# Kernel tuning notes

Measured on AMD Instinct MI355X. Metric: run time of the kernel, lower is better.

The kernel has to match this reference:

```python
import jax, jax.numpy as jnp
import numpy as np

BN_EPS = 1e-5
ITER_N = 5

def _bn(x, gamma, beta, mean, var, axis):
    shape = [1] * x.ndim
    shape[axis] = -1
    r = lambda v: v.reshape(shape)
    return (x - r(mean)) * (r(gamma) / jnp.sqrt(r(var) + BN_EPS)) + r(beta)

def _covpool(x):
    # x: (B, d, M); MPNCOV CovpoolLayer: y = x @ I_hat @ x^T, I_hat = (1/M)I - (1/M^2)11^T
    M = x.shape[-1]
    I_hat = (-1.0 / (M * M)) * jnp.ones((M, M), x.dtype) + (1.0 / M) * jnp.eye(M, dtype=x.dtype)
    return jnp.einsum('bdm,mn,ben->bde', x, I_hat, x)

def _sqrtm_ns(A, iterN=ITER_N):
    # MPNCOV SqrtmLayer: trace-normalized Newton-Schulz iteration
    d = A.shape[-1]
    I3 = 3.0 * jnp.eye(d, dtype=A.dtype)
    normA = jnp.trace(A, axis1=1, axis2=2) / 3.0          # (B,)
    A_n = A / normA[:, None, None]
    ZY = 0.5 * (I3 - A_n)
    Y = A_n @ ZY
    Z = ZY
    for _ in range(iterN - 2):
        ZY = 0.5 * (I3 - Z @ Y)
        Y = Y @ ZY
        Z = ZY @ Z
    YZY = 0.5 * (Y @ (I3 - Z @ Y))
    return YZY * jnp.sqrt(normA)[:, None, None]

def setup_inputs() -> dict:
    key = jax.random.key(0)
    ks = jax.random.split(key, 12)
    B, C, H, W = 64, 1024, 16, 16
    D, R = 128, H * W  # att_dim, sp_reso
    return {
        'x': jax.random.normal(ks[0], (B, C, H, W), jnp.float32),
        'w_dr': jax.random.normal(ks[1], (D, C), jnp.float32) * 0.02,
        'b_dr': jax.random.normal(ks[2], (D,), jnp.float32) * 0.02,
        'bn1_gamma': jnp.ones((D,), jnp.float32),
        'bn1_beta': jnp.zeros((D,), jnp.float32),
        'bn1_mean': jax.random.normal(ks[3], (D,), jnp.float32) * 0.1,
        'bn1_var': jax.random.uniform(ks[4], (D,), jnp.float32, 0.5, 1.5),
        'bn2_gamma': jnp.ones((R,), jnp.float32),
        'bn2_beta': jnp.zeros((R,), jnp.float32),
        'bn2_mean': jax.random.normal(ks[5], (R,), jnp.float32) * 0.1,
        'bn2_var': jax.random.uniform(ks[6], (R,), jnp.float32, 0.5, 1.5),
        'rc_w': jax.random.normal(ks[7], (R,), jnp.float32) * 0.1 + 1.0,
        'rc_b': jax.random.normal(ks[8], (R,), jnp.float32) * 0.02,
        'fc_w': jax.random.normal(ks[9], (R, R * R), jnp.float32) * 0.004,
        'fc_b': jax.random.normal(ks[10], (R,), jnp.float32) * 0.02,
    }

def reference(x, w_dr, b_dr, bn1_gamma, bn1_beta, bn1_mean, bn1_var,
              bn2_gamma, bn2_beta, bn2_mean, bn2_var, rc_w, rc_b, fc_w, fc_b):
    B, C, H, W = x.shape
    # 1x1 dimension-reduction conv + BN + ReLU
    y = jnp.einsum('bchw,dc->bdhw', x, w_dr) + b_dr[None, :, None, None]
    y = jax.nn.relu(_bn(y, bn1_gamma, bn1_beta, bn1_mean, bn1_var, axis=1))
    # (B, D, HW) -> (B, HW, D): HW spatial positions as 'channels', D as samples
    y = y.reshape(B, -1, H * W).transpose(0, 2, 1)
    cov = _covpool(y)                  # (B, HW, HW)
    s = _sqrtm_ns(cov, ITER_N)         # (B, HW, HW)
    # row BN over first HW axis (channels of the (B, HW, HW, 1) view)
    s = _bn(s, bn2_gamma, bn2_beta, bn2_mean, bn2_var, axis=1)
    # grouped (depthwise) 1x1 row conv: per-row scale + bias
    s = s * rc_w[None, :, None] + rc_b[None, :, None]
    att = jax.nn.sigmoid(s.reshape(B, -1) @ fc_w.T + fc_b)   # (B, HW)
    att = att.reshape(B, 1, H, W)
    return x * att
```

## Files before the change

kernel.cpp:

```cpp
#include <hip/hip_runtime.h>

typedef unsigned short u16;
typedef unsigned int   u32;
typedef __attribute__((ext_vector_type(8))) short bf8;
typedef __attribute__((ext_vector_type(4))) float f4;
typedef __attribute__((ext_vector_type(16))) float f16f;

#define MFMA(a,b,c)   __builtin_amdgcn_mfma_f32_16x16x32_bf16(a,b,c,0,0,0)
#define MFMA32(a,b,c) __builtin_amdgcn_mfma_f32_32x32x16_bf16(a,b,c,0,0,0)

__device__ __forceinline__ u16 f2bf(float f){
  u32 u = __float_as_uint(f);
  u += 0x7fffu + ((u >> 16) & 1u);
  return (u16)(u >> 16);
}
__device__ __forceinline__ float bf2f(u16 h){ return __uint_as_float(((u32)h) << 16); }
__device__ __forceinline__ u32 pk2(float a, float b){ return (u32)f2bf(a) | ((u32)f2bf(b) << 16); }

__device__ __forceinline__ void glds16(const u16* g, u16* l){
  __builtin_amdgcn_global_load_lds((const __attribute__((address_space(1))) u32*)g,
                                   (__attribute__((address_space(3))) u32*)l, 16, 0, 0);
}

__device__ __forceinline__ bf8 ldsFrag(const char* m, int row0, int k0, int pitch){
  int l = threadIdx.x & 63;
  int r = row0 + (l & 15);
  int kb = ((k0 + ((l >> 4) << 3)) << 1) ^ ((r & 7) << 4);
  return *(const bf8*)(m + r * pitch + kb);
}
__device__ __forceinline__ void ldsPut(char* m, int row, int col, int pitch, u16 v){
  int kb = (col << 1) ^ ((row & 7) << 4);
  *(u16*)(m + row * pitch + kb) = v;
}

__device__ __forceinline__ bf8 fragNS(const char* m, int r0, int ks, int l){
  int r = r0 + (l & 31);
  int kb = ((ks << 5) + ((l >> 5) << 4)) ^ ((r & 15) << 4);
  return *(const bf8*)(m + r * 256 + kb);
}
__device__ __forceinline__ bf8 fragWT(const char* m, int r0, int ks, int l){
  int r = r0 + (l & 31);
  int kb = ((ks << 5) + ((l >> 5) << 4)) ^ ((r & 15) << 4);
  return *(const bf8*)(m + r * 512 + kb);
}
__device__ __forceinline__ char* nsAddr(char* m, int row, int col4){
  return m + row * 256 + ((col4 << 1) ^ ((row & 15) << 4));
}

__device__ __forceinline__ void mmPass(const char* A, const char* B, f16f (&acc)[2][2],
                                       int R0, int C0, int l){
  #pragma unroll
  for (int ks = 0; ks < 8; ++ks){
    bf8 a0 = fragNS(A, R0,      ks, l);
    bf8 a1 = fragNS(A, R0 + 32, ks, l);
    bf8 b0 = fragNS(B, C0,      ks, l);
    bf8 b1 = fragNS(B, C0 + 32, ks, l);
    acc[0][0] = MFMA32(a0, b0, acc[0][0]); acc[0][1] = MFMA32(a0, b1, acc[0][1]);
    acc[1][0] = MFMA32(a1, b0, acc[1][0]); acc[1][1] = MFMA32(a1, b1, acc[1][1]);
  }
}

__device__ __forceinline__ void writeTile(char* D, const f16f (&acc)[2][2], int R0, int C0, int l,
                                          float scale, float dval, const uint2* adv){
  #pragma unroll
  for (int ri = 0; ri < 2; ++ri)
  #pragma unroll
  for (int ci = 0; ci < 2; ++ci)
  #pragma unroll
  for (int g = 0; g < 4; ++g){
    int srow = C0 + ci * 32 + (l & 31);
    int scol = R0 + ri * 32 + g * 8 + ((l >> 5) << 2);
    float v[4];
    #pragma unroll
    for (int q = 0; q < 4; ++q){
      float x = scale * acc[ri][ci][g * 4 + q];
      x += ((scol + q) == srow) ? dval : 0.f;
      v[q] = x;
    }
    if (adv){
      uint2 ad = adv[(ri * 2 + ci) * 4 + g];
      v[0] += 1.5f * bf2f((u16)ad.x);
      v[1] += 1.5f * bf2f((u16)(ad.x >> 16));
      v[2] += 1.5f * bf2f((u16)ad.y);
      v[3] += 1.5f * bf2f((u16)(ad.y >> 16));
    }
    *(uint2*)nsAddr(D, srow, scol) = make_uint2(pk2(v[0], v[1]), pk2(v[2], v[3]));
  }
}

__global__ __launch_bounds__(256) void k_prep(const float* __restrict__ wdr,
                                              float* __restrict__ logits,
                                              u16* __restrict__ prep){
  int i = blockIdx.x * 256 + threadIdx.x;
  if (i < 16384) logits[i] = 0.f;
  #pragma unroll
  for (int j = 0; j < 2; ++j){
    int e = i + j * 65536;
    int chunk = e >> 13, rem = e & 8191, d = rem >> 6, cb2 = rem & 63;
    int c = ((cb2 * 2) ^ ((d & 7) << 4)) >> 1;
    prep[e] = f2bf(wdr[d * 1024 + chunk * 64 + c]);
  }
}

__global__ __launch_bounds__(512) void k_conv(
    const u16* __restrict__ wprep, const float* __restrict__ x, const float* __restrict__ bdr,
    const float* __restrict__ g1, const float* __restrict__ be1,
    const float* __restrict__ m1, const float* __restrict__ v1,
    u16* __restrict__ Wg, u16* __restrict__ WTg){
  __shared__ union {
    struct { u16 A[2][8192]; u16 Bt[2][2048]; } s;
    struct { float y[128 * 33]; float musum[512]; float mu[32]; } e;
  } sm;
  int t = threadIdx.x;
  int b = blockIdx.x >> 3, hw0 = (blockIdx.x & 7) * 32;
  const float* xb = x + (size_t)b * 262144 + hw0;

  int w = t >> 6, l = t & 63;
  int d0 = (w >> 1) * 32, hh = (w & 1) * 16;
  int lc = l & 15, lr = (l >> 4) * 4;

  const f4 fz = {0.f, 0.f, 0.f, 0.f};
  f4 acc[2]; acc[0] = fz; acc[1] = fz;

  int cp = t >> 5, hwl = t & 31;
  int bo0 = (4 * cp) ^ ((hwl & 7) << 4);
  int bo1 = (4 * cp + 64) ^ ((hwl & 7) << 4);

  glds16(wprep + t * 8,        sm.s.A[0] + t * 8);
  glds16(wprep + 4096 + t * 8, sm.s.A[0] + 4096 + t * 8);
  glds16(wprep + 8192 + t * 8,        sm.s.A[1] + t * 8);
  glds16(wprep + 8192 + 4096 + t * 8, sm.s.A[1] + 4096 + t * 8);
  float br0 = xb[(size_t)(2 * cp)      * 256 + hwl];
  float br1 = xb[(size_t)(2 * cp + 1)  * 256 + hwl];
  float br2 = xb[(size_t)(2 * cp + 32) * 256 + hwl];
  float br3 = xb[(size_t)(2 * cp + 33) * 256 + hwl];

  #pragma unroll
  for (int k = 0; k < 16; ++k){
    if (k >= 1 && k < 15){
      const u16* src = wprep + (k + 1) * 8192;
      glds16(src + t * 8,        sm.s.A[(k + 1) & 1] + t * 8);
      glds16(src + 4096 + t * 8, sm.s.A[(k + 1) & 1] + 4096 + t * 8);
    }
    float nb0 = 0.f, nb1 = 0.f, nb2 = 0.f, nb3 = 0.f;
    if (k < 15){
      int c0 = (k + 1) * 64;
      nb0 = xb[(size_t)(c0 + 2 * cp)      * 256 + hwl];
      nb1 = xb[(size_t)(c0 + 2 * cp + 1)  * 256 + hwl];
      nb2 = xb[(size_t)(c0 + 2 * cp + 32) * 256 + hwl];
      nb3 = xb[(size_t)(c0 + 2 * cp + 33) * 256 + hwl];
    }
    __builtin_amdgcn_sched_barrier(0);
    if (k == 0)       asm volatile("s_waitcnt vmcnt(4)" ::: "memory");
    else if (k == 15) asm volatile("s_waitcnt vmcnt(0)" ::: "memory");
    else              asm volatile("s_waitcnt vmcnt(6)" ::: "memory");
    __builtin_amdgcn_sched_barrier(0);
    *(u32*)((char*)sm.s.Bt[k & 1] + hwl * 128 + bo0) = pk2(br0, br1);
    *(u32*)((char*)sm.s.Bt[k & 1] + hwl * 128 + bo1) = pk2(br2, br3);
    asm volatile("s_waitcnt lgkmcnt(0)" ::: "memory");
    __builtin_amdgcn_sched_barrier(0);
    __builtin_amdgcn_s_barrier();
    __builtin_amdgcn_sched_barrier(0);
    #pragma unroll
    for (int ks = 0; ks < 2; ++ks){
      int k0 = ks * 32;
      bf8 a0 = ldsFrag((const char*)sm.s.A[k & 1], d0,      k0, 128);
      bf8 a1 = ldsFrag((const char*)sm.s.A[k & 1], d0 + 16, k0, 128);
      bf8 b0 = ldsFrag((const char*)sm.s.Bt[k & 1], hh, k0, 128);
      acc[0] = MFMA(a0, b0, acc[0]);
      acc[1] = MFMA(a1, b0, acc[1]);
    }
    __builtin_amdgcn_sched_barrier(0);
    __builtin_amdgcn_s_barrier();
    __builtin_amdgcn_sched_barrier(0);
    br0 = nb0; br1 = nb1; br2 = nb2; br3 = nb3;
  }
  __syncthreads();

  #pragma unroll
  for (int i = 0; i < 2; ++i)
    #pragma unroll
    for (int r = 0; r < 4; ++r){
      int d = d0 + i * 16 + lr + r;
      float s1 = g1[d] * rsqrtf(v1[d] + 1e-5f);
      float t1 = (bdr[d] - m1[d]) * s1 + be1[d];
      int hwp = hh + lc;
      sm.e.y[d * 33 + hwp] = fmaxf(acc[i][r] * s1 + t1, 0.f);
    }
  __syncthreads();
  { int part = t >> 5, col = t & 31;
    float s = 0.f;
    #pragma unroll
    for (int i2 = 0; i2 < 8; ++i2) s += sm.e.y[(part * 8 + i2) * 33 + col];
    sm.e.musum[part * 32 + col] = s;
  }
  __syncthreads();
  if (t < 32){
    float m = 0.f;
    #pragma unroll
    for (int p = 0; p < 16; ++p) m += sm.e.musum[p * 32 + t];
    sm.e.mu[t] = m * (1.0f / 128.0f);
  }
  __syncthreads();
  const float ISM = 0.08838834764831845f;
  { int hwp = t >> 4, dc = (t & 15) * 8;
    float muv = sm.e.mu[hwp];
    u32 q[4];
    #pragma unroll
    for (int jj = 0; jj < 4; ++jj){
      float a = (sm.e.y[(dc + 2 * jj)     * 33 + hwp] - muv) * ISM;
      float c = (sm.e.y[(dc + 2 * jj + 1) * 33 + hwp] - muv) * ISM;
      q[jj] = pk2(a, c);
    }
    *(uint4*)(Wg + ((size_t)(b * 256 + hw0 + hwp) * 128 + dc)) = make_uint4(q[0], q[1], q[2], q[3]);
  }
  { int d = t >> 2, hc = (t & 3) * 8;
    u32 q[4];
    #pragma unroll
    for (int jj = 0; jj < 4; ++jj){
      int h0 = hc + 2 * jj, h1 = hc + 2 * jj + 1;
      float a = (sm.e.y[d * 33 + h0] - sm.e.mu[h0]) * ISM;
      float c = (sm.e.y[d * 33 + h1] - sm.e.mu[h1]) * ISM;
      q[jj] = pk2(a, c);
    }
    *(uint4*)(WTg + ((size_t)(b * 128 + d) * 256 + hw0 + hc)) = make_uint4(q[0], q[1], q[2], q[3]);
  }
}

extern __shared__ char smns[];
__global__ __launch_bounds__(512, 2) void k_ns(const u16* __restrict__ WT,
                                               u16* __restrict__ yf, float* __restrict__ normAg){
  int b = blockIdx.x, t = threadIdx.x;
  char* Yb = smns;
  char* Zb = smns + 32768;
  char* T1 = smns + 65536;
  char* T2 = smns + 98304;
  char* T3 = smns + 131072;
  char* WTl = smns + 65536;
  char* G   = T3;
  float* trp = (float*)smns;

  int w = t >> 6, l = t & 63;
  int wq = w & 3;
  int R0 = (wq >> 1) * 64, C0 = (wq & 1) * 64;

  { const u16* src = WT + (size_t)b * 32768;
    int row = t >> 2, q = t & 3;
    #pragma unroll
    for (int j = 0; j < 8; ++j) {
      int c16 = q + j * 4;
      bf8 v = *(const bf8*)(src + row * 256 + c16 * 8);
      int ph = c16 ^ (row & 15);
      *(bf8*)(WTl + row * 512 + ph * 16) = v;
    }
  }
  if (t == 0) *trp = 0.f;
  __syncthreads();

  int R0g = (w & 3) * 32, C0g = (w >> 2) * 64;
  const f16f fz16 = {};
  f16f gac[2]; gac[0] = fz16; gac[1] = fz16;
  #pragma unroll
  for (int ks = 0; ks < 16; ++ks){
    bf8 a  = fragWT(WTl, R0g,      ks, l);
    bf8 b0 = fragWT(WTl, C0g,      ks, l);
    bf8 b1 = fragWT(WTl, C0g + 32, ks, l);
    gac[0] = MFMA32(a, b0, gac[0]);
    gac[1] = MFMA32(a, b1, gac[1]);
  }
  float tp = 0.f;
  #pragma unroll
  for (int ci = 0; ci < 2; ++ci)
    #pragma unroll
    for (int e = 0; e < 16; ++e){
      int row = R0g + (e & 3) + 8 * (e >> 2) + ((l >> 5) << 2);
      int col = C0g + ci * 32 + (l & 31);
      if (row == col) tp += gac[ci][e];
    }
  #pragma unroll
  for (int off = 32; off > 0; off >>= 1) tp += __shfl_down(tp, off);
  if (l == 0) atomicAdd(trp, tp);
  __syncthreads();

  float normA = fmaxf(*trp / 3.0f, 1e-12f);
  if (t == 0) normAg[b] = normA;
  float inv = 1.0f / normA;
  #pragma unroll
  for (int ci = 0; ci < 2; ++ci)
    #pragma unroll
    for (int g = 0; g < 4; ++g){
      int srow = C0g + ci * 32 + (l & 31);
      int scol = R0g + g * 8 + ((l >> 5) << 2);
      float v0 = gac[ci][g * 4 + 0] * inv, v1 = gac[ci][g * 4 + 1] * inv;
      float v2 = gac[ci][g * 4 + 2] * inv, v3 = gac[ci][g * 4 + 3] * inv;
      *(uint2*)nsAddr(G, srow, scol) = make_uint2(pk2(v0, v1), pk2(v2, v3));
    }
  __syncthreads();

  bf8 gA[8], gB[8];
  #pragma unroll
  for (int ks = 0; ks < 8; ++ks){
    gA[ks] = fragNS(G, C0,      ks, l);
    gB[ks] = fragNS(G, C0 + 32, ks, l);
  }
  { int row = t >> 2, q4 = t & 3;
    #pragma unroll
    for (int j = 0; j < 4; ++j){
      int c16 = q4 * 4 + j;
      int ph = c16 ^ (row & 15);
      bf8 gg = *(const bf8*)(G + row * 256 + ph * 16);
      bf8 yv, zv;
      #pragma unroll
      for (int e = 0; e < 8; ++e){
        int col = c16 * 8 + e;
        float y = -0.5f * bf2f((u16)gg[e]) + ((col == row) ? 1.5f : 0.f);
        yv[e] = (short)f2bf(y);
        zv[e] = (col == row) ? (short)f2bf(-0.5f) : (short)0;
      }
      *(bf8*)(Yb + row * 256 + ph * 16) = yv;
      *(bf8*)(Zb + row * 256 + ph * 16) = zv;
    }
  }
  __syncthreads();

  float z0 = 1.5f;
  for (int it = 0; it < 4; ++it){
    {
      f16f acc[2][2]; acc[0][0] = fz16; acc[0][1] = fz16; acc[1][0] = fz16; acc[1][1] = fz16;
      const char* As = (w < 4) ? Zb : Yb;
      #pragma unroll
      for (int ks = 0; ks < 8; ++ks){
        bf8 a0 = fragNS(As, R0,      ks, l);
        bf8 a1 = fragNS(As, R0 + 32, ks, l);
        acc[0][0] = MFMA32(a0, gA[ks], acc[0][0]); acc[0][1] = MFMA32(a0, gB[ks], acc[0][1]);
        acc[1][0] = MFMA32(a1, gA[ks], acc[1][0]); acc[1][1] = MFMA32(a1, gB[ks], acc[1][1]);
      }
      writeTile((w < 4) ? T1 : T3, acc, R0, C0, l, 1.0f, (w < 4) ? z0 : 0.f, nullptr);
    }
    __syncthreads();

    uint2 adv[16];
    {
      const char* addsrc = (w < 4) ? Zb : Yb;
      #pragma unroll
      for (int ri = 0; ri < 2; ++ri)
      #pragma unroll
      for (int ci = 0; ci < 2; ++ci)
      #pragma unroll
      for (int g = 0; g < 4; ++g){
        int srow = C0 + ci * 32 + (l & 31);
        int scol = R0 + ri * 32 + g * 8 + ((l >> 5) << 2);
        adv[(ri * 2 + ci) * 4 + g] = *(const uint2*)nsAddr((char*)addsrc, srow, scol);
      }
      if (w < 4){
        f16f acc[2][2]; acc[0][0] = fz16; acc[0][1] = fz16; acc[1][0] = fz16; acc[1][1] = fz16;
        mmPass(T1, Yb, acc, R0, C0, l);
        writeTile(T2, acc, R0, C0, l, -0.5f, 0.f, nullptr);
      }
    }
    __syncthreads();

    if ((w >= 4) || (it < 3)){
      f16f acc[2][2]; acc[0][0] = fz16; acc[0][1] = fz16; acc[1][0] = fz16; acc[1][1] = fz16;
      const char* A3 = (w < 4) ? T2 : T3;
      const char* B3 = (w < 4) ? T1 : T2;
      mmPass(A3, B3, acc, R0, C0, l);
      writeTile((w < 4) ? Zb : Yb, acc, R0, C0, l, 1.0f, 0.f, adv);
    }
    __syncthreads();
    z0 *= 1.5f;
  }

  { int row = t >> 2, q = t & 3;
    u16* dst = yf + (size_t)b * 16384 + row * 128;
    #pragma unroll
    for (int j = 0; j < 4; ++j) {
      int c16 = q * 4 + j;
      int ph = c16 ^ (row & 15);
      *(bf8*)(dst + c16 * 8) = *(const bf8*)(Yb + row * 256 + ph * 16);
    }
  }
}

extern __shared__ char smex[];
__global__ __launch_bounds__(512) void k_expand(
    const u16* __restrict__ Wg, const u16* __restrict__ yf, const float* __restrict__ normAg,
    const float* __restrict__ g2, const float* __restrict__ be2, const float* __restrict__ m2,
    const float* __restrict__ v2, const float* __restrict__ rcw, const float* __restrict__ rcb,
    u16* __restrict__ sp){
  int blk = blockIdx.x, b = blk >> 2, iband = blk & 3;
  char* Bm = smex;
  char* Yl = smex + 65536;
  char* El = smex + 98304;
  int t = threadIdx.x;
  { const u16* src = Wg + (size_t)b * 32768;
    int row = t >> 1, q = t & 1;
    #pragma unroll
    for (int j = 0; j < 8; ++j) {
      int c16 = q + j * 2;
      bf8 v = *(const bf8*)(src + row * 128 + c16 * 8);
      int ph = c16 ^ (row & 7);
      *(bf8*)(Bm + row * 256 + ph * 16) = v;
    } }
  { const u16* src = yf + (size_t)b * 16384;
    int row = t >> 2, q = t & 3;
    #pragma unroll
    for (int j = 0; j < 4; ++j) {
      int c16 = q + j * 4;
      bf8 v = *(const bf8*)(src + row * 128 + c16 * 8);
      int ph = c16 ^ (row & 7);
      *(bf8*)(Yl + row * 256 + ph * 16) = v;
    } }
  __syncthreads();
  int w = t >> 6, l = t & 63, lc = l & 15, lr = (l >> 4) * 4;
  const f4 fz = {0.f, 0.f, 0.f, 0.f};
  { int r0 = (w >> 2) * 32, c0 = (w & 3) * 32;
    f4 acc[2][2];
    acc[0][0] = fz; acc[0][1] = fz; acc[1][0] = fz; acc[1][1] = fz;
    #pragma unroll
    for (int kk = 0; kk < 4; ++kk) {
      int k0 = kk * 32;
      bf8 a0 = ldsFrag(Bm, iband * 64 + r0,      k0, 256);
      bf8 a1 = ldsFrag(Bm, iband * 64 + r0 + 16, k0, 256);
      bf8 b0 = ldsFrag(Yl, c0,      k0, 256);
      bf8 b1 = ldsFrag(Yl, c0 + 16, k0, 256);
      acc[0][0] = MFMA(a0, b0, acc[0][0]); acc[0][1] = MFMA(a0, b1, acc[0][1]);
      acc[1][0] = MFMA(a1, b0, acc[1][0]); acc[1][1] = MFMA(a1, b1, acc[1][1]);
    }
    #pragma unroll
    for (int i = 0; i < 2; ++i)
      #pragma unroll
      for (int j = 0; j < 2; ++j)
        #pragma unroll
        for (int r = 0; r < 4; ++r)
          ldsPut(El, r0 + i * 16 + lr + r, c0 + j * 16 + lc, 256, f2bf(acc[i][j][r]));
  }
  __syncthreads();
  { float invs = rsqrtf(normAg[b]);
    int r0 = (w >> 2) * 32, c0 = (w & 3) * 64;
    f4 acc[2][4];
    #pragma unroll
    for (int i = 0; i < 2; ++i)
      #pragma unroll
      for (int j = 0; j < 4; ++j) acc[i][j] = fz;
    #pragma unroll
    for (int kk = 0; kk < 4; ++kk) {
      int k0 = kk * 32;
      bf8 a0 = ldsFrag(El, r0,      k0, 256);
      bf8 a1 = ldsFrag(El, r0 + 16, k0, 256);
      bf8 b0 = ldsFrag(Bm, c0,      k0, 256);
      bf8 b1 = ldsFrag(Bm, c0 + 16, k0, 256);
      bf8 b2 = ldsFrag(Bm, c0 + 32, k0, 256);
      bf8 b3 = ldsFrag(Bm, c0 + 48, k0, 256);
      acc[0][0] = MFMA(a0, b0, acc[0][0]); acc[0][1] = MFMA(a0, b1, acc[0][1]);
      acc[0][2] = MFMA(a0, b2, acc[0][2]); acc[0][3] = MFMA(a0, b3, acc[0][3]);
      acc[1][0] = MFMA(a1, b0, acc[1][0]); acc[1][1] = MFMA(a1, b1, acc[1][1]);
      acc[1][2] = MFMA(a1, b2, acc[1][2]); acc[1][3] = MFMA(a1, b3, acc[1][3]);
    }
    #pragma unroll
    for (int i = 0; i < 2; ++i)
      #pragma unroll
      for (int r = 0; r < 4; ++r) {
        int il = r0 + i * 16 + lr + r;
        int ig = iband * 64 + il;
        float bs = g2[ig] * rsqrtf(v2[ig] + 1e-5f);
        float al = bs * rcw[ig];
        float be = (be2[ig] - m2[ig] * bs) * rcw[ig] + rcb[ig];
        #pragma unroll
        for (int j = 0; j < 4; ++j) {
          int jg = c0 + j * 16 + lc;
          sp[(size_t)b * 65536 + ig * 256 + jg] = f2bf(acc[i][j][r] * invs * al + be);
        }
      }
  }
}

__global__ __launch_bounds__(256) void k_fc(const u16* __restrict__ sp,
                                            const float* __restrict__ fcw,
                                            float* __restrict__ partial){
  __shared__ char Bl[2][16384];
  int kc = blockIdx.x >> 2, rq = blockIdx.x & 3;
  int t = threadIdx.x, w = t >> 6, l = t & 63;
  int k0 = kc * 512, rbase = rq * 64;
  int br0 = (w & 1) * 32;
  int cr0 = (w >> 1) * 32;

  const f4 fz = {0.f, 0.f, 0.f, 0.f};
  f4 acc[2][2];
  acc[0][0] = fz; acc[0][1] = fz; acc[1][0] = fz; acc[1][1] = fz;

  float4 fbA[8], fbB[8];
  bf8 faA[8], faB[8];

  #define LOADB(S, FB) { \
    _Pragma("unroll") \
    for (int j = 0; j < 8; ++j){ \
      int fid = t + 256 * j; \
      int row = fid >> 5, c4 = fid & 31; \
      FB[j] = *(const float4*)(fcw + (size_t)(rbase + row) * 65536 + k0 + (S) * 128 + c4 * 4); \
    } }
  #define LOADA(S, FA) { \
    _Pragma("unroll") \
    for (int g = 0; g < 2; ++g) \
    _Pragma("unroll") \
    for (int ks = 0; ks < 4; ++ks) \
      FA[g * 4 + ks] = *(const bf8*)(sp + (size_t)(br0 + 16 * g + (l & 15)) * 65536 \
                                     + k0 + (S) * 128 + ks * 32 + (l >> 4) * 8); \
    }
  #define WRITEB(CUR, FB) { \
    _Pragma("unroll") \
    for (int j = 0; j < 8; ++j){ \
      int fid = t + 256 * j; \
      int row = fid >> 5, c4 = fid & 31; \
      int off = row * 256 + ((c4 * 8) ^ ((row & 7) << 4)); \
      *(uint2*)(&Bl[CUR][0] + off) = make_uint2(pk2(FB[j].x, FB[j].y), pk2(FB[j].z, FB[j].w)); \
    } }
  #define DOMFMA(CUR, FA) { \
    _Pragma("unroll") \
    for (int ks = 0; ks < 4; ++ks){ \
      bf8 b0 = ldsFrag(&Bl[CUR][0], cr0,      ks * 32, 256); \
      bf8 b1 = ldsFrag(&Bl[CUR][0], cr0 + 16, ks * 32, 256); \
      acc[0][0] = MFMA(FA[ks],     b0, acc[0][0]); \
      acc[0][1] = MFMA(FA[ks],     b1, acc[0][1]); \
      acc[1][0] = MFMA(FA[4 + ks], b0, acc[1][0]); \
      acc[1][1] = MFMA(FA[4 + ks], b1, acc[1][1]); \
    } }
  #define FENCE __builtin_amdgcn_sched_barrier(0)
  #define BARRIER { FENCE; __builtin_amdgcn_s_barrier(); FENCE; }

  LOADB(0, fbA); LOADA(0, faA);
  LOADB(1, fbB); LOADA(1, faB);

  FENCE; asm volatile("s_waitcnt vmcnt(16)" ::: "memory"); FENCE;
  WRITEB(0, fbA);
  asm volatile("s_waitcnt lgkmcnt(0)" ::: "memory");
  BARRIER;
  DOMFMA(0, faA);
  LOADB(2, fbA); LOADA(2, faA);
  BARRIER;
  FENCE; asm volatile("s_waitcnt vmcnt(16)" ::: "memory"); FENCE;
  WRITEB(1, fbB);
  asm volatile("s_waitcnt lgkmcnt(0)" ::: "memory");
  BARRIER;
  DOMFMA(1, faB);
  LOADB(3, fbB); LOADA(3, faB);
  BARRIER;
  FENCE; asm volatile("s_waitcnt vmcnt(16)" ::: "memory"); FENCE;
  WRITEB(0, fbA);
  asm volatile("s_waitcnt lgkmcnt(0)" ::: "memory");
  BARRIER;
  DOMFMA(0, faA);
  BARRIER;
  FENCE; asm volatile("s_waitcnt vmcnt(0)" ::: "memory"); FENCE;
  WRITEB(1, fbB);
  asm volatile("s_waitcnt lgkmcnt(0)" ::: "memory");
  BARRIER;
  DOMFMA(1, faB);

  #undef LOADB
  #undef LOADA
  #undef WRITEB
  #undef DOMFMA
  #undef FENCE
  #undef BARRIER

  float* pout = partial + (size_t)kc * 16384;
  #pragma unroll
  for (int g = 0; g < 2; ++g)
    #pragma unroll
    for (int j = 0; j < 2; ++j)
      #pragma unroll
      for (int q = 0; q < 4; ++q){
        int brow = br0 + g * 16 + ((l >> 4) << 2) + q;
        int rcol = rbase + cr0 + j * 16 + (l & 15);
        pout[brow * 256 + rcol] = acc[g][j][q];
      }
}

__global__ __launch_bounds__(256) void k_red(const float* __restrict__ partial,
                                             float* __restrict__ logits){
  int i = blockIdx.x * 256 + threadIdx.x;
  float s0 = 0.f, s1 = 0.f, s2 = 0.f, s3 = 0.f;
  #pragma unroll 8
  for (int kc = 0; kc < 128; kc += 4){
    s0 += partial[(size_t)(kc + 0) * 16384 + i];
    s1 += partial[(size_t)(kc + 1) * 16384 + i];
    s2 += partial[(size_t)(kc + 2) * 16384 + i];
    s3 += partial[(size_t)(kc + 3) * 16384 + i];
  }
  logits[i] = (s0 + s1) + (s2 + s3);
}

__global__ __launch_bounds__(256) void k_mul(const float* __restrict__ x,
                                             const float* __restrict__ logits,
                                             const float* __restrict__ fcb,
                                             float* __restrict__ out, int n4){
  int i = blockIdx.x * 256 + threadIdx.x;
  int str = gridDim.x * 256;
  for (; i < n4; i += str) {
    int e = i << 2;
    int b = e >> 18;
    int hw = e & 255;
    float4 xv = ((const float4*)x)[i];
    float4 lg = *(const float4*)(logits + (b << 8) + hw);
    float4 fb = *(const float4*)(fcb + hw);
    float4 o;
    o.x = xv.x / (1.f + expf(-(lg.x + fb.x)));
    o.y = xv.y / (1.f + expf(-(lg.y + fb.y)));
    o.z = xv.z / (1.f + expf(-(lg.z + fb.z)));
    o.w = xv.w / (1.f + expf(-(lg.w + fb.w)));
    ((float4*)out)[i] = o;
  }
}

extern "C" void kernel_launch(void* const* d_in, const int* in_sizes, int n_in,
                              void* d_out, int out_size, void* d_ws, size_t ws_size,
                              hipStream_t stream){
  const float* x   = (const float*)d_in[0];
  const float* wdr = (const float*)d_in[1];
  const float* bdr = (const float*)d_in[2];
  const float* g1  = (const float*)d_in[3];
  const float* be1 = (const float*)d_in[4];
  const float* m1  = (const float*)d_in[5];
  const float* v1  = (const float*)d_in[6];
  const float* g2  = (const float*)d_in[7];
  const float* be2 = (const float*)d_in[8];
  const float* m2  = (const float*)d_in[9];
  const float* v2  = (const float*)d_in[10];
  const float* rcw = (const float*)d_in[11];
  const float* rcb = (const float*)d_in[12];
  const float* fcw = (const float*)d_in[13];
  const float* fcb = (const float*)d_in[14];
  float* out = (float*)d_out;
  char* ws = (char*)d_ws;
  u16*   Wg  = (u16*)(ws);
  u16*   WTg = (u16*)(ws + (4u  << 20));
  u16*   yfg = (u16*)(ws + (8u  << 20));
  float* nAg = (float*)(ws + (10u << 20));
  u16*   wpr = (u16*)(ws + (10u << 20) + 4096);
  u16*   spg = (u16*)(ws + (11u << 20));
  float* lgt = (float*)(ws + (20u << 20));
  float* prt = (float*)(ws + (24u << 20));

  hipFuncSetAttribute((const void*)k_ns,     hipFuncAttributeMaxDynamicSharedMemorySize, 163840);
  hipFuncSetAttribute((const void*)k_expand, hipFuncAttributeMaxDynamicSharedMemorySize, 114688);

  k_prep  <<<256,  256, 0,      stream>>>(wdr, lgt, wpr);
  k_conv  <<<512,  512, 0,      stream>>>(wpr, x, bdr, g1, be1, m1, v1, Wg, WTg);
  k_ns    <<<64,   512, 163840, stream>>>(WTg, yfg, nAg);
  k_expand<<<256,  512, 114688, stream>>>(Wg, yfg, nAg, g2, be2, m2, v2, rcw, rcb, spg);
  k_fc    <<<512,  256, 0,      stream>>>(spg, fcw, prt);
  k_red   <<<64,   256, 0,      stream>>>(prt, lgt);
  k_mul   <<<2048, 256, 0,      stream>>>(x, lgt, fcb, out, 4194304);
}
```

Measured before the change: 115.3 us.

## Deepen conv weight/input prefetch pipeline and split NS matmul across all waves

The 1x1 conv kernel goes from a double-buffered weight stage to a four-slot LDS ring that prefetches three chunks ahead. The x-input register prefetch also moves to a three-deep rotation, so more global loads are in flight before each MFMA step; the vmcnt waits are retuned to match. In the Newton-Schulz kernel, the T1*Y product was computed only by waves 0-3. It is now split across all eight waves, each computing a 64x32 half-tile, which removes idle waves at that step. The cost is more LDS for the conv kernel, which may lower occupancy, and more live registers.

```diff
diff --git a/kernel.cpp b/kernel.cpp
--- a/kernel.cpp
+++ b/kernel.cpp
@@ -108,7 +108,7 @@
     const float* __restrict__ m1, const float* __restrict__ v1,
     u16* __restrict__ Wg, u16* __restrict__ WTg){
   __shared__ union {
-    struct { u16 A[2][8192]; u16 Bt[2][2048]; } s;
+    struct { u16 A[4][8192]; u16 Bt[2][2048]; } s;
     struct { float y[128 * 33]; float musum[512]; float mu[32]; } e;
   } sm;
   int t = threadIdx.x;
@@ -126,37 +126,44 @@
   int bo0 = (4 * cp) ^ ((hwl & 7) << 4);
   int bo1 = (4 * cp + 64) ^ ((hwl & 7) << 4);
 
-  glds16(wprep + t * 8,        sm.s.A[0] + t * 8);
-  glds16(wprep + 4096 + t * 8, sm.s.A[0] + 4096 + t * 8);
-  glds16(wprep + 8192 + t * 8,        sm.s.A[1] + t * 8);
-  glds16(wprep + 8192 + 4096 + t * 8, sm.s.A[1] + 4096 + t * 8);
-  float br0 = xb[(size_t)(2 * cp)      * 256 + hwl];
-  float br1 = xb[(size_t)(2 * cp + 1)  * 256 + hwl];
-  float br2 = xb[(size_t)(2 * cp + 32) * 256 + hwl];
-  float br3 = xb[(size_t)(2 * cp + 33) * 256 + hwl];
+  float br[3][4];
+  #pragma unroll
+  for (int j = 0; j < 3; ++j){
+    glds16(wprep + j * 8192 + t * 8,        sm.s.A[j] + t * 8);
+    glds16(wprep + j * 8192 + 4096 + t * 8, sm.s.A[j] + 4096 + t * 8);
+    __builtin_amdgcn_sched_barrier(0);
+    int c0 = j * 64;
+    br[j][0] = xb[(size_t)(c0 + 2 * cp)      * 256 + hwl];
+    br[j][1] = xb[(size_t)(c0 + 2 * cp + 1)  * 256 + hwl];
+    br[j][2] = xb[(size_t)(c0 + 2 * cp + 32) * 256 + hwl];
+    br[j][3] = xb[(size_t)(c0 + 2 * cp + 33) * 256 + hwl];
+    __builtin_amdgcn_sched_barrier(0);
+  }
 
   #pragma unroll
   for (int k = 0; k < 16; ++k){
-    if (k >= 1 && k < 15){
-      const u16* src = wprep + (k + 1) * 8192;
-      glds16(src + t * 8,        sm.s.A[(k + 1) & 1] + t * 8);
-      glds16(src + 4096 + t * 8, sm.s.A[(k + 1) & 1] + 4096 + t * 8);
-    }
-    float nb0 = 0.f, nb1 = 0.f, nb2 = 0.f, nb3 = 0.f;
-    if (k < 15){
-      int c0 = (k + 1) * 64;
-      nb0 = xb[(size_t)(c0 + 2 * cp)      * 256 + hwl];
-      nb1 = xb[(size_t)(c0 + 2 * cp + 1)  * 256 + hwl];
-      nb2 = xb[(size_t)(c0 + 2 * cp + 32) * 256 + hwl];
-      nb3 = xb[(size_t)(c0 + 2 * cp + 33) * 256 + hwl];
-    }
-    __builtin_amdgcn_sched_barrier(0);
-    if (k == 0)       asm volatile("s_waitcnt vmcnt(4)" ::: "memory");
-    else if (k == 15) asm volatile("s_waitcnt vmcnt(0)" ::: "memory");
-    else              asm volatile("s_waitcnt vmcnt(6)" ::: "memory");
-    __builtin_amdgcn_sched_barrier(0);
-    *(u32*)((char*)sm.s.Bt[k & 1] + hwl * 128 + bo0) = pk2(br0, br1);
-    *(u32*)((char*)sm.s.Bt[k & 1] + hwl * 128 + bo1) = pk2(br2, br3);
+    if (k <= 12){
+      const u16* src = wprep + (k + 3) * 8192;
+      glds16(src + t * 8,        sm.s.A[(k + 3) & 3] + t * 8);
+      glds16(src + 4096 + t * 8, sm.s.A[(k + 3) & 3] + 4096 + t * 8);
+    }
+    __builtin_amdgcn_sched_barrier(0);
+    if (k <= 12)      asm volatile("s_waitcnt vmcnt(14)" ::: "memory");
+    else if (k == 13) asm volatile("s_waitcnt vmcnt(12)" ::: "memory");
+    else if (k == 14) asm volatile("s_waitcnt vmcnt(6)" ::: "memory");
+    else              asm volatile("s_waitcnt vmcnt(0)" ::: "memory");
+    __builtin_amdgcn_sched_barrier(0);
+    *(u32*)((char*)sm.s.Bt[k & 1] + hwl * 128 + bo0) = pk2(br[k % 3][0], br[k % 3][1]);
+    *(u32*)((char*)sm.s.Bt[k & 1] + hwl * 128 + bo1) = pk2(br[k % 3][2], br[k % 3][3]);
+    __builtin_amdgcn_sched_barrier(0);
+    if (k <= 12){
+      int c0 = (k + 3) * 64;
+      br[k % 3][0] = xb[(size_t)(c0 + 2 * cp)      * 256 + hwl];
+      br[k % 3][1] = xb[(size_t)(c0 + 2 * cp + 1)  * 256 + hwl];
+      br[k % 3][2] = xb[(size_t)(c0 + 2 * cp + 32) * 256 + hwl];
+      br[k % 3][3] = xb[(size_t)(c0 + 2 * cp + 33) * 256 + hwl];
+    }
+    __builtin_amdgcn_sched_barrier(0);
     asm volatile("s_waitcnt lgkmcnt(0)" ::: "memory");
     __builtin_amdgcn_sched_barrier(0);
     __builtin_amdgcn_s_barrier();
@@ -164,8 +171,8 @@
     #pragma unroll
     for (int ks = 0; ks < 2; ++ks){
       int k0 = ks * 32;
-      bf8 a0 = ldsFrag((const char*)sm.s.A[k & 1], d0,      k0, 128);
-      bf8 a1 = ldsFrag((const char*)sm.s.A[k & 1], d0 + 16, k0, 128);
+      bf8 a0 = ldsFrag((const char*)sm.s.A[k & 3], d0,      k0, 128);
+      bf8 a1 = ldsFrag((const char*)sm.s.A[k & 3], d0 + 16, k0, 128);
       bf8 b0 = ldsFrag((const char*)sm.s.Bt[k & 1], hh, k0, 128);
       acc[0] = MFMA(a0, b0, acc[0]);
       acc[1] = MFMA(a1, b0, acc[1]);
@@ -173,7 +180,6 @@
     __builtin_amdgcn_sched_barrier(0);
     __builtin_amdgcn_s_barrier();
     __builtin_amdgcn_sched_barrier(0);
-    br0 = nb0; br1 = nb1; br2 = nb2; br3 = nb3;
   }
   __syncthreads();
 
@@ -352,10 +358,25 @@
         int scol = R0 + ri * 32 + g * 8 + ((l >> 5) << 2);
         adv[(ri * 2 + ci) * 4 + g] = *(const uint2*)nsAddr((char*)addsrc, srow, scol);
       }
-      if (w < 4){
-        f16f acc[2][2]; acc[0][0] = fz16; acc[0][1] = fz16; acc[1][0] = fz16; acc[1][1] = fz16;
-        mmPass(T1, Yb, acc, R0, C0, l);
-        writeTile(T2, acc, R0, C0, l, -0.5f, 0.f, nullptr);
+      int hC0 = C0 + ((w >> 2) << 5);
+      f16f a2[2]; a2[0] = fz16; a2[1] = fz16;
+      #pragma unroll
+      for (int ks = 0; ks < 8; ++ks){
+        bf8 a0 = fragNS(T1, R0,      ks, l);
+        bf8 a1 = fragNS(T1, R0 + 32, ks, l);
+        bf8 b0 = fragNS(Yb, hC0,     ks, l);
+        a2[0] = MFMA32(a0, b0, a2[0]);
+        a2[1] = MFMA32(a1, b0, a2[1]);
+      }
+      #pragma unroll
+      for (int ri = 0; ri < 2; ++ri)
+      #pragma unroll
+      for (int g = 0; g < 4; ++g){
+        int srow = hC0 + (l & 31);
+        int scol = R0 + ri * 32 + g * 8 + ((l >> 5) << 2);
+        float v0 = -0.5f * a2[ri][g * 4 + 0], v1 = -0.5f * a2[ri][g * 4 + 1];
+        float v2 = -0.5f * a2[ri][g * 4 + 2], v3 = -0.5f * a2[ri][g * 4 + 3];
+        *(uint2*)nsAddr(T2, srow, scol) = make_uint2(pk2(v0, v1), pk2(v2, v3));
       }
     }
     __syncthreads();
```

New measurement: 113.9 us. About the same (-1.2%).
